# Kernel optimization log

Hardware: AMD Instinct MI355X
Metric: run time of the kernel (lower is better)

The kernel has to match this reference:

```python
import jax, jax.numpy as jnp
import numpy as np

B, S, D_IN, R = 8, 4096, 2048, 64


def setup_inputs() -> dict:
    key = jax.random.key(0)
    kx, kw = jax.random.split(key)
    x = jax.random.normal(kx, (B, S, D_IN), dtype=jnp.float32)
    weight = jax.random.normal(kw, (B, D_IN, R), dtype=jnp.float32) * 0.02
    return {"x": x, "weight": weight}


def reference(x, weight):
    # Batched per-adapter LoRA matmul: [B,S,D] @ [B,D,R] -> [B,S,R]
    return jnp.einsum('bsd,bdr->bsr', x, weight)
```

## Files before the change

### kernel.cpp

```cpp
#include <hip/hip_runtime.h>
#include <hip/hip_bf16.h>

typedef __attribute__((ext_vector_type(8))) short short8;
typedef __attribute__((ext_vector_type(4))) float f32x4;

static constexpr int Bn = 8, Sn = 4096, Dn = 2048, Rn = 64;
static constexpr int BM = 64;
static constexpr int NCHUNK = Dn / 64;
static constexpr int WF_PER_B = NCHUNK * 4096;

__device__ __forceinline__ unsigned short f2bf(float f) {
    unsigned u = __builtin_bit_cast(unsigned, f);
    u += 0x7FFFu + ((u >> 16) & 1u);
    return (unsigned short)(u >> 16);
}
__device__ __forceinline__ float bf2f(unsigned short h) {
    unsigned u = (unsigned)h << 16;
    return __builtin_bit_cast(float, u);
}

__global__ __launch_bounds__(256) void prep_w(const float* __restrict__ W,
                                              unsigned short* __restrict__ Wf) {
    const int t    = blockIdx.x * 256 + threadIdx.x;
    const int lane = t & 63;
    const int nt   = (t >> 6) & 3;
    const int ks   = (t >> 8) & 1;
    const int c    = (t >> 9) & 31;
    const int b    = t >> 14;
    const int g    = lane >> 4;
    const int r    = nt * 16 + (lane & 15);
    const float* __restrict__ src =
        W + ((size_t)b * Dn + c * 64 + ks * 32 + g * 8) * Rn + r;
    short8 o;
#pragma unroll
    for (int f = 0; f < 8; ++f) o[f] = (short)f2bf(src[(size_t)f * Rn]);
    *reinterpret_cast<short8*>(Wf + (size_t)t * 8) = o;
}

struct ABuf { float4 v0, v1, v2, v3; };

__device__ __forceinline__ void load_a(ABuf& A, const float* p) {
    A.v0 = *reinterpret_cast<const float4*>(p);
    A.v1 = *reinterpret_cast<const float4*>(p + 4);
    A.v2 = *reinterpret_cast<const float4*>(p + 32);
    A.v3 = *reinterpret_cast<const float4*>(p + 36);
}
__device__ __forceinline__ void load_b(short8* Bv, const unsigned short* q) {
#pragma unroll
    for (int i = 0; i < 8; ++i)
        Bv[i] = *reinterpret_cast<const short8*>(q + i * 512);
}
__device__ __forceinline__ short8 cvt8(const float4& a, const float4& b) {
    short8 h;
    h[0] = (short)f2bf(a.x); h[1] = (short)f2bf(a.y);
    h[2] = (short)f2bf(a.z); h[3] = (short)f2bf(a.w);
    h[4] = (short)f2bf(b.x); h[5] = (short)f2bf(b.y);
    h[6] = (short)f2bf(b.z); h[7] = (short)f2bf(b.w);
    return h;
}
__device__ __forceinline__ void compute_chunk(const ABuf& A, const short8* Bv, f32x4* acc) {
    const short8 h0 = cvt8(A.v0, A.v1);
    const short8 h1 = cvt8(A.v2, A.v3);
#pragma unroll
    for (int nt = 0; nt < 4; ++nt)
        acc[nt] = __builtin_amdgcn_mfma_f32_16x16x32_bf16(h0, Bv[nt], acc[nt], 0, 0, 0);
#pragma unroll
    for (int nt = 0; nt < 4; ++nt)
        acc[nt] = __builtin_amdgcn_mfma_f32_16x16x32_bf16(h1, Bv[4 + nt], acc[nt], 0, 0, 0);
}

__global__ __launch_bounds__(256, 2)
void lora_main(const float* __restrict__ X, const unsigned short* __restrict__ Wf,
               float* __restrict__ O) {
    const int blk  = blockIdx.x;
    const int b    = blk >> 6;
    const int m0   = (blk & 63) * BM;
    const int tid  = threadIdx.x;
    const int wid  = tid >> 6;
    const int lane = tid & 63;
    const int l15  = lane & 15;
    const int g    = lane >> 4;

    const float* xp = X + (size_t)b * (Sn * Dn)
                        + (size_t)(m0 + wid * 16 + l15) * Dn + g * 8;
    const unsigned short* bp = Wf + (size_t)b * WF_PER_B + lane * 8;

    f32x4 acc[4];
#pragma unroll
    for (int i = 0; i < 4; ++i) acc[i] = f32x4{0.f, 0.f, 0.f, 0.f};

    ABuf A0, A1;
    short8 B0[8], B1[8];
    load_a(A0, xp);
    load_b(B0, bp);

    for (int c = 0; c < NCHUNK; c += 2) {
        load_a(A1, xp + 64);
        load_b(B1, bp + 4096);
        compute_chunk(A0, B0, acc);

        const bool last = (c + 2 >= NCHUNK);
        const float*          xp2 = last ? xp : (xp + 128);
        const unsigned short* bp2 = last ? bp : (bp + 8192);
        load_a(A0, xp2);
        load_b(B0, bp2);
        compute_chunk(A1, B1, acc);

        xp += 128;
        bp += 8192;
    }

    float* __restrict__ ob = O + (size_t)b * (Sn * Rn) + (size_t)(m0 + wid * 16) * Rn;
    const int r0 = g * 4;
#pragma unroll
    for (int nt = 0; nt < 4; ++nt) {
#pragma unroll
        for (int r = 0; r < 4; ++r) {
            ob[(size_t)(r0 + r) * Rn + nt * 16 + l15] = acc[nt][r];
        }
    }
}

__global__ __launch_bounds__(256, 2)
void batch_lora_fused(const float* __restrict__ X, const float* __restrict__ W,
                      float* __restrict__ O) {
    __shared__ unsigned short wlds[2 * 4 * 64 * 8];
    const int blk  = blockIdx.x;
    const int b    = blk >> 6;
    const int m0   = (blk & 63) * BM;
    const int tid  = threadIdx.x;
    const int wid  = tid >> 6;
    const int lane = tid & 63;
    const int l15  = lane & 15;
    const int g    = lane >> 4;
    const float* __restrict__ xrow = X + (size_t)b * (Sn * Dn)
                                       + (size_t)(m0 + wid * 16 + l15) * Dn + g * 8;
    const float* __restrict__ wb = W + (size_t)b * (Dn * Rn);
    f32x4 acc[4];
#pragma unroll
    for (int i = 0; i < 4; ++i) acc[i] = f32x4{0.f, 0.f, 0.f, 0.f};
    for (int kb = 0; kb < Dn; kb += 64) {
#pragma unroll
        for (int i = 0; i < 4; ++i) {
            const int e  = 4 * (tid + 256 * i);
            const int kk = e >> 6;
            const int cc = e & 63;
            const float4 w4 = *reinterpret_cast<const float4*>(
                wb + (size_t)(kb + kk) * Rn + cc);
            const int ks = kk >> 5;
            const int k5 = kk & 31;
            const int nt = cc >> 4;
            const int f  = k5 & 7;
            const int lw = 16 * (k5 >> 3) + (cc & 15);
            unsigned short* dst = &wlds[((ks * 4 + nt) * 64 + lw) * 8 + f];
            dst[0 * 8] = f2bf(w4.x); dst[1 * 8] = f2bf(w4.y);
            dst[2 * 8] = f2bf(w4.z); dst[3 * 8] = f2bf(w4.w);
        }
        __syncthreads();
#pragma unroll
        for (int ks = 0; ks < 2; ++ks) {
            const float* ap = xrow + kb + ks * 32;
            const float4 a0 = *reinterpret_cast<const float4*>(ap);
            const float4 a1 = *reinterpret_cast<const float4*>(ap + 4);
            const short8 ahi = cvt8(a0, a1);
#pragma unroll
            for (int nt = 0; nt < 4; ++nt) {
                const short8 bhi = *reinterpret_cast<const short8*>(
                    &wlds[((ks * 4 + nt) * 64 + lane) * 8]);
                acc[nt] = __builtin_amdgcn_mfma_f32_16x16x32_bf16(ahi, bhi, acc[nt], 0, 0, 0);
            }
        }
        __syncthreads();
    }
    float* __restrict__ ob = O + (size_t)b * (Sn * Rn) + (size_t)(m0 + wid * 16) * Rn;
    const int r0 = g * 4;
#pragma unroll
    for (int nt = 0; nt < 4; ++nt)
#pragma unroll
        for (int r = 0; r < 4; ++r)
            ob[(size_t)(r0 + r) * Rn + nt * 16 + l15] = acc[nt][r];
}

extern "C" void kernel_launch(void* const* d_in, const int* in_sizes, int n_in,
                              void* d_out, int out_size, void* d_ws, size_t ws_size,
                              hipStream_t stream) {
    const float* x = (const float*)d_in[0];
    const float* w = (const float*)d_in[1];
    float* out = (float*)d_out;
    const size_t wf_bytes = (size_t)Bn * WF_PER_B * sizeof(unsigned short);
    if (ws_size >= wf_bytes) {
        unsigned short* wf = (unsigned short*)d_ws;
        prep_w<<<dim3(512), dim3(256), 0, stream>>>(w, wf);
        lora_main<<<dim3(Bn * (Sn / BM)), dim3(256), 0, stream>>>(x, wf, out);
    } else {
        batch_lora_fused<<<dim3(Bn * (Sn / BM)), dim3(256), 0, stream>>>(x, w, out);
    }
}
```

Baseline: 68.00 us.

## Split output columns across wave pairs with smaller row tiles and higher occupancy

The main kernel now tiles 32 rows per block and gives each pair of waves the same 16 rows while splitting the 64 output columns in halves. That doubles the block count, halves the per-wave B-fragment registers and accumulators, and raises the launch-bounds occupancy hint from 2 to 4 blocks per CU. Each X row is now loaded and converted by two waves, so global/L2 traffic for the activation stream doubles (though L1/L2 may absorb some of it). The float-to-bf16 conversion also switches to the packed HIP intrinsic.

```diff
diff --git a/kernel.cpp b/kernel.cpp
--- a/kernel.cpp
+++ b/kernel.cpp
@@ -5,7 +5,6 @@
 typedef __attribute__((ext_vector_type(4))) float f32x4;
 
 static constexpr int Bn = 8, Sn = 4096, Dn = 2048, Rn = 64;
-static constexpr int BM = 64;
 static constexpr int NCHUNK = Dn / 64;
 static constexpr int WF_PER_B = NCHUNK * 4096;
 
@@ -13,10 +12,6 @@
     unsigned u = __builtin_bit_cast(unsigned, f);
     u += 0x7FFFu + ((u >> 16) & 1u);
     return (unsigned short)(u >> 16);
-}
-__device__ __forceinline__ float bf2f(unsigned short h) {
-    unsigned u = (unsigned)h << 16;
-    return __builtin_bit_cast(float, u);
 }
 
 __global__ __launch_bounds__(256) void prep_w(const float* __restrict__ W,
@@ -45,78 +40,88 @@
     A.v2 = *reinterpret_cast<const float4*>(p + 32);
     A.v3 = *reinterpret_cast<const float4*>(p + 36);
 }
-__device__ __forceinline__ void load_b(short8* Bv, const unsigned short* q) {
-#pragma unroll
-    for (int i = 0; i < 8; ++i)
-        Bv[i] = *reinterpret_cast<const short8*>(q + i * 512);
+__device__ __forceinline__ void load_b4(short8* Bv, const unsigned short* q) {
+    Bv[0] = *reinterpret_cast<const short8*>(q);
+    Bv[1] = *reinterpret_cast<const short8*>(q + 512);
+    Bv[2] = *reinterpret_cast<const short8*>(q + 2048);
+    Bv[3] = *reinterpret_cast<const short8*>(q + 2560);
 }
 __device__ __forceinline__ short8 cvt8(const float4& a, const float4& b) {
+    __hip_bfloat162 p0 = __float22bfloat162_rn(float2{a.x, a.y});
+    __hip_bfloat162 p1 = __float22bfloat162_rn(float2{a.z, a.w});
+    __hip_bfloat162 p2 = __float22bfloat162_rn(float2{b.x, b.y});
+    __hip_bfloat162 p3 = __float22bfloat162_rn(float2{b.z, b.w});
     short8 h;
-    h[0] = (short)f2bf(a.x); h[1] = (short)f2bf(a.y);
-    h[2] = (short)f2bf(a.z); h[3] = (short)f2bf(a.w);
-    h[4] = (short)f2bf(b.x); h[5] = (short)f2bf(b.y);
-    h[6] = (short)f2bf(b.z); h[7] = (short)f2bf(b.w);
+    h[0] = (short)__builtin_bit_cast(unsigned short, p0.x);
+    h[1] = (short)__builtin_bit_cast(unsigned short, p0.y);
+    h[2] = (short)__builtin_bit_cast(unsigned short, p1.x);
+    h[3] = (short)__builtin_bit_cast(unsigned short, p1.y);
+    h[4] = (short)__builtin_bit_cast(unsigned short, p2.x);
+    h[5] = (short)__builtin_bit_cast(unsigned short, p2.y);
+    h[6] = (short)__builtin_bit_cast(unsigned short, p3.x);
+    h[7] = (short)__builtin_bit_cast(unsigned short, p3.y);
     return h;
 }
 __device__ __forceinline__ void compute_chunk(const ABuf& A, const short8* Bv, f32x4* acc) {
     const short8 h0 = cvt8(A.v0, A.v1);
     const short8 h1 = cvt8(A.v2, A.v3);
-#pragma unroll
-    for (int nt = 0; nt < 4; ++nt)
-        acc[nt] = __builtin_amdgcn_mfma_f32_16x16x32_bf16(h0, Bv[nt], acc[nt], 0, 0, 0);
-#pragma unroll
-    for (int nt = 0; nt < 4; ++nt)
-        acc[nt] = __builtin_amdgcn_mfma_f32_16x16x32_bf16(h1, Bv[4 + nt], acc[nt], 0, 0, 0);
-}
-
-__global__ __launch_bounds__(256, 2)
+    acc[0] = __builtin_amdgcn_mfma_f32_16x16x32_bf16(h0, Bv[0], acc[0], 0, 0, 0);
+    acc[1] = __builtin_amdgcn_mfma_f32_16x16x32_bf16(h0, Bv[1], acc[1], 0, 0, 0);
+    acc[0] = __builtin_amdgcn_mfma_f32_16x16x32_bf16(h1, Bv[2], acc[0], 0, 0, 0);
+    acc[1] = __builtin_amdgcn_mfma_f32_16x16x32_bf16(h1, Bv[3], acc[1], 0, 0, 0);
+}
+
+__global__ __launch_bounds__(256, 4)
 void lora_main(const float* __restrict__ X, const unsigned short* __restrict__ Wf,
                float* __restrict__ O) {
     const int blk  = blockIdx.x;
-    const int b    = blk >> 6;
-    const int m0   = (blk & 63) * BM;
+    const int b    = blk >> 7;
+    const int m0   = (blk & 127) * 32;
     const int tid  = threadIdx.x;
     const int wid  = tid >> 6;
     const int lane = tid & 63;
     const int l15  = lane & 15;
     const int g    = lane >> 4;
+    const int wrow = (wid >> 1) * 16;
+    const int wnt  = (wid & 1) * 2;
 
     const float* xp = X + (size_t)b * (Sn * Dn)
-                        + (size_t)(m0 + wid * 16 + l15) * Dn + g * 8;
-    const unsigned short* bp = Wf + (size_t)b * WF_PER_B + lane * 8;
-
-    f32x4 acc[4];
-#pragma unroll
-    for (int i = 0; i < 4; ++i) acc[i] = f32x4{0.f, 0.f, 0.f, 0.f};
+                        + (size_t)(m0 + wrow + l15) * Dn + g * 8;
+    const unsigned short* bp = Wf + (size_t)b * WF_PER_B + wnt * 512 + lane * 8;
+
+    f32x4 acc[2];
+    acc[0] = f32x4{0.f, 0.f, 0.f, 0.f};
+    acc[1] = f32x4{0.f, 0.f, 0.f, 0.f};
 
     ABuf A0, A1;
-    short8 B0[8], B1[8];
+    short8 B0[4], B1[4];
     load_a(A0, xp);
-    load_b(B0, bp);
+    load_b4(B0, bp);
 
     for (int c = 0; c < NCHUNK; c += 2) {
         load_a(A1, xp + 64);
-        load_b(B1, bp + 4096);
+        load_b4(B1, bp + 4096);
         compute_chunk(A0, B0, acc);
 
         const bool last = (c + 2 >= NCHUNK);
         const float*          xp2 = last ? xp : (xp + 128);
         const unsigned short* bp2 = last ? bp : (bp + 8192);
         load_a(A0, xp2);
-        load_b(B0, bp2);
+        load_b4(B0, bp2);
         compute_chunk(A1, B1, acc);
 
         xp += 128;
         bp += 8192;
     }
 
-    float* __restrict__ ob = O + (size_t)b * (Sn * Rn) + (size_t)(m0 + wid * 16) * Rn;
+    float* __restrict__ ob = O + (size_t)b * (Sn * Rn) + (size_t)(m0 + wrow) * Rn;
     const int r0 = g * 4;
 #pragma unroll
-    for (int nt = 0; nt < 4; ++nt) {
+    for (int i = 0; i < 2; ++i) {
+        const int col = (wnt + i) * 16 + l15;
 #pragma unroll
         for (int r = 0; r < 4; ++r) {
-            ob[(size_t)(r0 + r) * Rn + nt * 16 + l15] = acc[nt][r];
+            ob[(size_t)(r0 + r) * Rn + col] = acc[i][r];
         }
     }
 }
@@ -127,7 +132,7 @@
     __shared__ unsigned short wlds[2 * 4 * 64 * 8];
     const int blk  = blockIdx.x;
     const int b    = blk >> 6;
-    const int m0   = (blk & 63) * BM;
+    const int m0   = (blk & 63) * 64;
     const int tid  = threadIdx.x;
     const int wid  = tid >> 6;
     const int lane = tid & 63;
@@ -191,8 +196,8 @@
     if (ws_size >= wf_bytes) {
         unsigned short* wf = (unsigned short*)d_ws;
         prep_w<<<dim3(512), dim3(256), 0, stream>>>(w, wf);
-        lora_main<<<dim3(Bn * (Sn / BM)), dim3(256), 0, stream>>>(x, wf, out);
+        lora_main<<<dim3(Bn * (Sn / 32)), dim3(256), 0, stream>>>(x, wf, out);
     } else {
-        batch_lora_fused<<<dim3(Bn * (Sn / BM)), dim3(256), 0, stream>>>(x, w, out);
-    }
-}
+        batch_lora_fused<<<dim3(Bn * (Sn / 64)), dim3(256), 0, stream>>>(x, w, out);
+    }
+}
```

Result: slower. 96.82 us (+42.4%).
